# Optimization experiments

Hardware: AMD Instinct MI355X
Metric: run time of the kernel (lower is better)

Reference implementation:

```python
import jax, jax.numpy as jnp
import numpy as np
import math

N, IN_DIM, OUT_DIM = 4096, 1024, 1024
MASK = True


def setup_inputs() -> dict:
    key = jax.random.key(0)
    ks = jax.random.split(key, 6)
    s = 1.0 / math.sqrt(IN_DIM)
    return {
        "qx": jax.random.normal(ks[0], (N, IN_DIM), jnp.float32),
        "kx": jax.random.normal(ks[1], (N, IN_DIM), jnp.float32),
        "vx": jax.random.normal(ks[2], (N, IN_DIM), jnp.float32),
        # torch nn.Linear weight layout: [out_dim, in_dim], y = x @ W.T
        "Wq": jax.random.normal(ks[3], (OUT_DIM, IN_DIM), jnp.float32) * s,
        "Wk": jax.random.normal(ks[4], (OUT_DIM, IN_DIM), jnp.float32) * s,
        "Wv": jax.random.normal(ks[5], (OUT_DIM, IN_DIM), jnp.float32) * s,
    }


def reference(qx, kx, vx, Wq, Wk, Wv):
    q = qx @ Wq.T  # [n, d]
    k = kx @ Wk.T
    v = vx @ Wv.T
    scores = (q @ k.T) / jnp.float32(math.sqrt(OUT_DIM))  # [n, n]
    if MASK:
        n = qx.shape[0]
        col = jnp.arange(n)[None, :]
        row = jnp.arange(n)[:, None]
        # original: -10000 where j > i (strictly upper triangular)
        scores = scores + jnp.where(col > row, jnp.float32(-10000.0), jnp.float32(0.0))
    attn = jax.nn.softmax(scores, axis=1)
    return attn @ v
```

## Files before the change

### kernel.cpp

```cpp
#include <hip/hip_runtime.h>
#include <hip/hip_bf16.h>
#include <stdint.h>

#define NTOK 4096
#define DIM  1024

typedef unsigned short u16;
typedef __bf16 bf16x8 __attribute__((ext_vector_type(8)));
typedef float f32x4 __attribute__((ext_vector_type(4)));
typedef u16 u16x8 __attribute__((ext_vector_type(8)));

__device__ __forceinline__ u16 f2bf(float f) {
  union { float f; uint32_t u; } c; c.f = f;
  return (u16)((c.u + 0x7fffu + ((c.u >> 16) & 1u)) >> 16);
}
__device__ __forceinline__ float bf2f(u16 b) {
  union { uint32_t u; float f; } c; c.u = (uint32_t)b << 16;
  return c.f;
}

__device__ __forceinline__ float wave_max(float v) {
#pragma unroll
  for (int o = 32; o; o >>= 1) v = fmaxf(v, __shfl_xor(v, o, 64));
  return v;
}
__device__ __forceinline__ float wave_sum(float v) {
#pragma unroll
  for (int o = 32; o; o >>= 1) v += __shfl_xor(v, o, 64);
  return v;
}

__device__ __forceinline__ int xcd_swz(int orig, int nwg) {
  const int q = nwg >> 3, r = nwg & 7;
  const int x = orig & 7, i = orig >> 3;
  return (x < r ? x * (q + 1) : r * (q + 1) + (x - r) * q) + i;
}

__device__ __forceinline__ void gld16(const u16* g, u16* l) {
  __builtin_amdgcn_global_load_lds((const __attribute__((address_space(1))) void*)g,
                                   (__attribute__((address_space(3))) void*)l, 16, 0, 0);
}

__global__ __launch_bounds__(256) void cvt6(
    const float* __restrict__ qx, const float* __restrict__ kx, const float* __restrict__ vx,
    const float* __restrict__ Wq, const float* __restrict__ Wk, const float* __restrict__ Wv,
    u16* __restrict__ qxb, u16* __restrict__ kxb, u16* __restrict__ vxb,
    u16* __restrict__ Wqb, u16* __restrict__ Wkb, u16* __restrict__ Wvb)
{
  const int z = blockIdx.z;
  const int nelem = (z < 3) ? NTOK * DIM : DIM * DIM;
  const int i = (blockIdx.x * 256 + threadIdx.x) * 8;
  if (i >= nelem) return;
  const float* in = (z == 0) ? qx : (z == 1) ? kx : (z == 2) ? vx
                  : (z == 3) ? Wq : (z == 4) ? Wk : Wv;
  u16* out = (z == 0) ? qxb : (z == 1) ? kxb : (z == 2) ? vxb
           : (z == 3) ? Wqb : (z == 4) ? Wkb : Wvb;
  float4 a = *reinterpret_cast<const float4*>(in + i);
  float4 b = *reinterpret_cast<const float4*>(in + i + 4);
  u16x8 o;
  o[0] = f2bf(a.x); o[1] = f2bf(a.y); o[2] = f2bf(a.z); o[3] = f2bf(a.w);
  o[4] = f2bf(b.x); o[5] = f2bf(b.y); o[6] = f2bf(b.z); o[7] = f2bf(b.w);
  *reinterpret_cast<u16x8*>(out + i) = o;
}

template<int BM>
__device__ __forceinline__ void mm_core(
    const u16* __restrict__ A, const u16* __restrict__ B,
    int lda, int ldb, int klo, int khi, int row0, int col0,
    u16* sA, u16* sB, f32x4 (&acc)[BM / 32][4])
{
  constexpr int RPWA = BM / 4;
  constexpr int ASZ = BM * 64;
  constexpr int BSZ = 128 * 64;
  const int tid = threadIdx.x;
  const int wave = tid >> 6, lane = tid & 63;
  const int wr = wave >> 1, wc = wave & 1;
  const int l15 = lane & 15, l4 = lane >> 4;
  const int h = l15 & 7;

  const int r8 = lane >> 3;
  const int scol = ((lane & 7) ^ r8) << 3;
  const u16* gA = A + (size_t)(row0 + wave * RPWA + r8) * lda + scol;
  const u16* gB = B + (size_t)(col0 + wave * 32 + r8) * ldb + scol;
  const int lbA = wave * RPWA * 64;
  const int lbB = wave * 32 * 64;

#pragma unroll
  for (int i = 0; i < RPWA / 8; ++i)
    gld16(gA + (size_t)(i * 8) * lda + klo, &sA[lbA + i * 512]);
#pragma unroll
  for (int i = 0; i < 4; ++i)
    gld16(gB + (size_t)(i * 8) * ldb + klo, &sB[lbB + i * 512]);
  __syncthreads();

  int cur = 0;
  for (int k0 = klo; k0 < khi; k0 += 64) {
    const int nxt = cur ^ 1;
    if (k0 + 64 < khi) {
#pragma unroll
      for (int i = 0; i < RPWA / 8; ++i)
        gld16(gA + (size_t)(i * 8) * lda + k0 + 64, &sA[nxt * ASZ + lbA + i * 512]);
#pragma unroll
      for (int i = 0; i < 4; ++i)
        gld16(gB + (size_t)(i * 8) * ldb + k0 + 64, &sB[nxt * BSZ + lbB + i * 512]);
    }
    const char* bA = (const char*)(sA + cur * ASZ);
    const char* bB = (const char*)(sB + cur * BSZ);
#pragma unroll
    for (int ks = 0; ks < 2; ++ks) {
      bf16x8 af[BM / 32], bfv[4];
#pragma unroll
      for (int mf = 0; mf < BM / 32; ++mf)
        af[mf] = *reinterpret_cast<const bf16x8*>(
            bA + ((wr * (BM / 2) + mf * 16 + l15) << 7) + ((((ks << 2) + l4) ^ h) << 4));
#pragma unroll
      for (int nf = 0; nf < 4; ++nf)
        bfv[nf] = *reinterpret_cast<const bf16x8*>(
            bB + ((wc * 64 + nf * 16 + l15) << 7) + ((((ks << 2) + l4) ^ h) << 4));
#pragma unroll
      for (int mf = 0; mf < BM / 32; ++mf)
#pragma unroll
        for (int nf = 0; nf < 4; ++nf)
          acc[mf][nf] = __builtin_amdgcn_mfma_f32_16x16x32_bf16(af[mf], bfv[nf], acc[mf][nf], 0, 0, 0);
    }
    __syncthreads();
    cur = nxt;
  }
}

__global__ __launch_bounds__(256) void proj_sw(
    const u16* __restrict__ qxb, const u16* __restrict__ kxb, const u16* __restrict__ vxb,
    const u16* __restrict__ Wqb, const u16* __restrict__ Wkb, const u16* __restrict__ Wvb,
    u16* __restrict__ qb, u16* __restrict__ kb, u16* __restrict__ vT)
{
  __shared__ alignas(16) u16 sA[2 * 128 * 64];
  __shared__ alignas(16) u16 sB[2 * 128 * 64];
  const int w = xcd_swz(blockIdx.x, 768);
  const int z = w >> 8, rem = w & 255;
  const int by = rem >> 3, bx = rem & 7;
  const u16* A = (z == 0) ? qxb : (z == 1) ? kxb : vxb;
  const u16* B = (z == 0) ? Wqb : (z == 1) ? Wkb : Wvb;
  const int row0 = by * 128, col0 = bx * 128;

  f32x4 acc[4][4] = {};
  mm_core<128>(A, B, DIM, DIM, 0, DIM, row0, col0, sA, sB, acc);

  const int lane = threadIdx.x & 63;
  const int wave = threadIdx.x >> 6;
  const int l15 = lane & 15, l4 = lane >> 4;
  const int om = row0 + (wave >> 1) * 64;
  const int on = col0 + (wave & 1) * 64;
  if (z < 2) {
    u16* C = (z == 0) ? qb : kb;
#pragma unroll
    for (int mf = 0; mf < 4; ++mf)
#pragma unroll
      for (int nf = 0; nf < 4; ++nf)
#pragma unroll
        for (int r = 0; r < 4; ++r)
          C[(size_t)(om + mf * 16 + l4 * 4 + r) * DIM + (on + nf * 16 + l15)] = f2bf(acc[mf][nf][r]);
  } else {
#pragma unroll
    for (int mf = 0; mf < 4; ++mf)
#pragma unroll
      for (int nf = 0; nf < 4; ++nf) {
        ushort4 o;
        o.x = f2bf(acc[mf][nf][0]);
        o.y = f2bf(acc[mf][nf][1]);
        o.z = f2bf(acc[mf][nf][2]);
        o.w = f2bf(acc[mf][nf][3]);
        *reinterpret_cast<ushort4*>(&vT[(size_t)(on + nf * 16 + l15) * NTOK + (om + mf * 16 + l4 * 4)]) = o;
      }
  }
}

__global__ __launch_bounds__(256) void gemm_scores(
    const u16* __restrict__ A, const u16* __restrict__ B, u16* __restrict__ C, float scale)
{
  __shared__ alignas(16) u16 sA[2 * 128 * 64];
  __shared__ alignas(16) u16 sB[2 * 128 * 64];
  const int t = xcd_swz(blockIdx.x, 528);
  int by = (int)((sqrtf(8.0f * t + 1.0f) - 1.0f) * 0.5f);
  while ((by + 1) * (by + 2) / 2 <= t) ++by;
  while (by * (by + 1) / 2 > t) --by;
  const int bx = t - by * (by + 1) / 2;
  const int row0 = by * 128, col0 = bx * 128;

  f32x4 acc[4][4] = {};
  mm_core<128>(A, B, DIM, DIM, 0, DIM, row0, col0, sA, sB, acc);

  const int lane = threadIdx.x & 63;
  const int wave = threadIdx.x >> 6;
  const int l15 = lane & 15, l4 = lane >> 4;
  const int om = row0 + (wave >> 1) * 64;
  const int on = col0 + (wave & 1) * 64;
#pragma unroll
  for (int mf = 0; mf < 4; ++mf)
#pragma unroll
    for (int nf = 0; nf < 4; ++nf)
#pragma unroll
      for (int r = 0; r < 4; ++r)
        C[(size_t)(om + mf * 16 + l4 * 4 + r) * NTOK + (on + nf * 16 + l15)] = f2bf(acc[mf][nf][r] * scale);
}

__global__ __launch_bounds__(256) void gemm_pv(
    const u16* __restrict__ P, const u16* __restrict__ vT, float* __restrict__ C)
{
  __shared__ alignas(16) u16 sA[2 * 64 * 64];
  __shared__ alignas(16) u16 sB[2 * 128 * 64];
  const int w = xcd_swz(blockIdx.x, 768);
  const int bx = w & 7;
  const int cid = w >> 3;
  int by, half;
  if (cid < 32) { by = cid; half = -1; }
  else { const int j = cid - 32; by = 32 + (j >> 1); half = j & 1; }
  const int row0 = by * 64, col0 = bx * 128;
  const int Klim = row0 + 64;
  int klo = 0, khi = Klim;
  if (half >= 0) {
    const int h1 = (((Klim >> 6) + 1) >> 1) << 6;
    if (half == 0) khi = h1; else klo = h1;
  }

  f32x4 acc[2][4] = {};
  mm_core<64>(P, vT, NTOK, NTOK, klo, khi, row0, col0, sA, sB, acc);

  const int lane = threadIdx.x & 63;
  const int wave = threadIdx.x >> 6;
  const int l15 = lane & 15, l4 = lane >> 4;
  const int om = row0 + (wave >> 1) * 32;
  const int on = col0 + (wave & 1) * 64;
#pragma unroll
  for (int mf = 0; mf < 2; ++mf)
#pragma unroll
    for (int nf = 0; nf < 4; ++nf)
#pragma unroll
      for (int r = 0; r < 4; ++r) {
        const size_t idx = (size_t)(om + mf * 16 + l4 * 4 + r) * DIM + (on + nf * 16 + l15);
        if (half >= 0) atomicAdd(&C[idx], acc[mf][nf][r]);
        else C[idx] = acc[mf][nf][r];
      }
}

__global__ __launch_bounds__(256) void softmax_causal(const u16* __restrict__ S,
                                                      u16* __restrict__ P) {
  __shared__ float buf[NTOK];
  __shared__ float red[8];
  const int row = blockIdx.x;
  const int tid = threadIdx.x;
  const int limit = row + 1;
  const int limit128 = (row & ~127) + 128;
  const u16* srow = S + (size_t)row * NTOK;

  float lmax = -1e30f;
  for (int j = tid * 8; j < limit128; j += 2048) {
    float v[8];
    if (j + 8 <= limit) {
      u16x8 sv = *reinterpret_cast<const u16x8*>(srow + j);
#pragma unroll
      for (int e = 0; e < 8; ++e) v[e] = bf2f(sv[e]);
    } else {
#pragma unroll
      for (int e = 0; e < 8; ++e) v[e] = (j + e < limit) ? bf2f(srow[j + e]) : -1e30f;
    }
    float4 lo = {v[0], v[1], v[2], v[3]}, hi = {v[4], v[5], v[6], v[7]};
    *reinterpret_cast<float4*>(buf + j) = lo;
    *reinterpret_cast<float4*>(buf + j + 4) = hi;
#pragma unroll
    for (int e = 0; e < 8; ++e) lmax = fmaxf(lmax, v[e]);
  }
  lmax = wave_max(lmax);
  if ((tid & 63) == 0) red[tid >> 6] = lmax;
  __syncthreads();
  const float m = fmaxf(fmaxf(red[0], red[1]), fmaxf(red[2], red[3]));

  float lsum = 0.f;
  for (int j = tid * 8; j < limit128; j += 2048) {
    float4 lo = *reinterpret_cast<float4*>(buf + j);
    float4 hi = *reinterpret_cast<float4*>(buf + j + 4);
    float e0 = __expf(lo.x - m), e1 = __expf(lo.y - m), e2 = __expf(lo.z - m), e3 = __expf(lo.w - m);
    float e4 = __expf(hi.x - m), e5 = __expf(hi.y - m), e6 = __expf(hi.z - m), e7 = __expf(hi.w - m);
    float4 eo = {e0, e1, e2, e3}, eh = {e4, e5, e6, e7};
    *reinterpret_cast<float4*>(buf + j) = eo;
    *reinterpret_cast<float4*>(buf + j + 4) = eh;
    lsum += ((e0 + e1) + (e2 + e3)) + ((e4 + e5) + (e6 + e7));
  }
  lsum = wave_sum(lsum);
  if ((tid & 63) == 0) red[4 + (tid >> 6)] = lsum;
  __syncthreads();
  const float inv = 1.0f / (red[4] + red[5] + red[6] + red[7]);

  u16* prow = P + (size_t)row * NTOK;
  for (int j = tid * 8; j < limit128; j += 2048) {
    float4 lo = *reinterpret_cast<float4*>(buf + j);
    float4 hi = *reinterpret_cast<float4*>(buf + j + 4);
    u16x8 o;
    o[0] = f2bf(lo.x * inv); o[1] = f2bf(lo.y * inv);
    o[2] = f2bf(lo.z * inv); o[3] = f2bf(lo.w * inv);
    o[4] = f2bf(hi.x * inv); o[5] = f2bf(hi.y * inv);
    o[6] = f2bf(hi.z * inv); o[7] = f2bf(hi.w * inv);
    *reinterpret_cast<u16x8*>(prow + j) = o;
  }
}

extern "C" void kernel_launch(void* const* d_in, const int* in_sizes, int n_in,
                              void* d_out, int out_size, void* d_ws, size_t ws_size,
                              hipStream_t stream) {
  const float* qx = (const float*)d_in[0];
  const float* kx = (const float*)d_in[1];
  const float* vx = (const float*)d_in[2];
  const float* Wq = (const float*)d_in[3];
  const float* Wk = (const float*)d_in[4];
  const float* Wv = (const float*)d_in[5];
  float* out = (float*)d_out;
  char* ws = (char*)d_ws;
  const size_t MB = 1024ull * 1024ull;

  if (ws_size < 120 * MB) {
    hipMemsetAsync(d_out, 0xFF, (size_t)out_size * sizeof(float), stream);
    return;
  }

  u16* qxb = (u16*)(ws);
  u16* kxb = (u16*)(ws + 8 * MB);
  u16* vxb = (u16*)(ws + 16 * MB);
  u16* Wqb = (u16*)(ws + 24 * MB);
  u16* Wkb = (u16*)(ws + 26 * MB);
  u16* Wvb = (u16*)(ws + 28 * MB);
  u16* S   = (u16*)(ws);
  u16* qb  = (u16*)(ws + 64 * MB);
  u16* kb  = (u16*)(ws + 72 * MB);
  u16* vT  = (u16*)(ws + 80 * MB);
  u16* P   = (u16*)(ws + 88 * MB);

  hipMemsetAsync((char*)out + (size_t)2048 * DIM * 4, 0, (size_t)2048 * DIM * 4, stream);

  cvt6<<<dim3(NTOK * DIM / (256 * 8), 1, 6), 256, 0, stream>>>(
      qx, kx, vx, Wq, Wk, Wv, qxb, kxb, vxb, Wqb, Wkb, Wvb);

  proj_sw<<<768, 256, 0, stream>>>(qxb, kxb, vxb, Wqb, Wkb, Wvb, qb, kb, vT);

  gemm_scores<<<528, 256, 0, stream>>>(qb, kb, S, 0.03125f);

  softmax_causal<<<NTOK, 256, 0, stream>>>(S, P);

  gemm_pv<<<768, 256, 0, stream>>>(P, vT, out);
}
```

Measured before the change: 140.5 us.

## Switch GEMM mainloop to 3-stage K=32 pipeline with vmcnt-based waits

```diff
diff --git a/kernel.cpp b/kernel.cpp
--- a/kernel.cpp
+++ b/kernel.cpp
@@ -39,6 +39,14 @@
 __device__ __forceinline__ void gld16(const u16* g, u16* l) {
   __builtin_amdgcn_global_load_lds((const __attribute__((address_space(1))) void*)g,
                                    (__attribute__((address_space(3))) void*)l, 16, 0, 0);
+}
+
+template<int N> __device__ __forceinline__ void wait_vmcnt() {
+  if constexpr (N == 0) asm volatile("s_waitcnt vmcnt(0)" ::: "memory");
+  else if constexpr (N == 3) asm volatile("s_waitcnt vmcnt(3)" ::: "memory");
+  else if constexpr (N == 4) asm volatile("s_waitcnt vmcnt(4)" ::: "memory");
+  else if constexpr (N == 6) asm volatile("s_waitcnt vmcnt(6)" ::: "memory");
+  else if constexpr (N == 8) asm volatile("s_waitcnt vmcnt(8)" ::: "memory");
 }
 
 __global__ __launch_bounds__(256) void cvt6(
@@ -67,64 +75,72 @@
 __device__ __forceinline__ void mm_core(
     const u16* __restrict__ A, const u16* __restrict__ B,
     int lda, int ldb, int klo, int khi, int row0, int col0,
-    u16* sA, u16* sB, f32x4 (&acc)[BM / 32][4])
-{
-  constexpr int RPWA = BM / 4;
-  constexpr int ASZ = BM * 64;
-  constexpr int BSZ = 128 * 64;
+    u16* lds, f32x4 (&acc)[BM / 32][4])
+{
+  constexpr int ABUF = BM * 32;
+  constexpr int BUFSZ = ABUF + 128 * 32;
+  constexpr int RPW_A = BM / 4;
+  constexpr int LPS = BM / 64 + 2;
   const int tid = threadIdx.x;
   const int wave = tid >> 6, lane = tid & 63;
   const int wr = wave >> 1, wc = wave & 1;
   const int l15 = lane & 15, l4 = lane >> 4;
-  const int h = l15 & 7;
-
-  const int r8 = lane >> 3;
-  const int scol = ((lane & 7) ^ r8) << 3;
-  const u16* gA = A + (size_t)(row0 + wave * RPWA + r8) * lda + scol;
-  const u16* gB = B + (size_t)(col0 + wave * 32 + r8) * ldb + scol;
-  const int lbA = wave * RPWA * 64;
-  const int lbB = wave * 32 * 64;
-
-#pragma unroll
-  for (int i = 0; i < RPWA / 8; ++i)
-    gld16(gA + (size_t)(i * 8) * lda + klo, &sA[lbA + i * 512]);
-#pragma unroll
-  for (int i = 0; i < 4; ++i)
-    gld16(gB + (size_t)(i * 8) * ldb + klo, &sB[lbB + i * 512]);
-  __syncthreads();
+
+  const int srow = lane >> 2;
+  const int gchunk = ((lane & 3) ^ ((lane >> 3) & 3)) << 3;
+  const u16* gA = A + (size_t)(row0 + wave * RPW_A + srow) * lda + gchunk;
+  const u16* gB = B + (size_t)(col0 + wave * 32 + srow) * ldb + gchunk;
+  const int lbA = wave * RPW_A * 32;
+  const int lbB = ABUF + wave * 32 * 32;
+
+  const int nsteps = (khi - klo) >> 5;
+
+  auto stage = [&](int s, u16* buf) {
+    const int k = klo + (s << 5);
+#pragma unroll
+    for (int i = 0; i < RPW_A / 16; ++i)
+      gld16(gA + (size_t)(i * 16) * lda + k, buf + lbA + i * 16 * 32);
+#pragma unroll
+    for (int i = 0; i < 2; ++i)
+      gld16(gB + (size_t)(i * 16) * ldb + k, buf + lbB + i * 16 * 32);
+  };
+
+  if (0 < nsteps) stage(0, lds);
+  if (1 < nsteps) stage(1, lds + BUFSZ);
+  if (2 < nsteps) stage(2, lds + 2 * BUFSZ);
 
   int cur = 0;
-  for (int k0 = klo; k0 < khi; k0 += 64) {
-    const int nxt = cur ^ 1;
-    if (k0 + 64 < khi) {
-#pragma unroll
-      for (int i = 0; i < RPWA / 8; ++i)
-        gld16(gA + (size_t)(i * 8) * lda + k0 + 64, &sA[nxt * ASZ + lbA + i * 512]);
-#pragma unroll
-      for (int i = 0; i < 4; ++i)
-        gld16(gB + (size_t)(i * 8) * ldb + k0 + 64, &sB[nxt * BSZ + lbB + i * 512]);
+  for (int t = 0; t < nsteps; ++t) {
+    const int ahead = nsteps - 1 - t;
+    if (ahead >= 2)      wait_vmcnt<2 * LPS>();
+    else if (ahead == 1) wait_vmcnt<LPS>();
+    else                 wait_vmcnt<0>();
+    __builtin_amdgcn_s_barrier();
+    __builtin_amdgcn_sched_barrier(0);
+    const char* buf = (const char*)(lds + cur * BUFSZ);
+
+    bf16x8 af[BM / 32], bfv[4];
+#pragma unroll
+    for (int mf = 0; mf < BM / 32; ++mf) {
+      const int r = wr * (BM / 2) + mf * 16 + l15;
+      af[mf] = *reinterpret_cast<const bf16x8*>(
+          buf + (r << 6) + (((l4 ^ (r >> 1)) & 3) << 4));
     }
-    const char* bA = (const char*)(sA + cur * ASZ);
-    const char* bB = (const char*)(sB + cur * BSZ);
-#pragma unroll
-    for (int ks = 0; ks < 2; ++ks) {
-      bf16x8 af[BM / 32], bfv[4];
-#pragma unroll
-      for (int mf = 0; mf < BM / 32; ++mf)
-        af[mf] = *reinterpret_cast<const bf16x8*>(
-            bA + ((wr * (BM / 2) + mf * 16 + l15) << 7) + ((((ks << 2) + l4) ^ h) << 4));
+#pragma unroll
+    for (int nf = 0; nf < 4; ++nf) {
+      const int r = wc * 64 + nf * 16 + l15;
+      bfv[nf] = *reinterpret_cast<const bf16x8*>(
+          buf + 2 * ABUF + (r << 6) + (((l4 ^ (r >> 1)) & 3) << 4));
+    }
+#pragma unroll
+    for (int mf = 0; mf < BM / 32; ++mf)
 #pragma unroll
       for (int nf = 0; nf < 4; ++nf)
-        bfv[nf] = *reinterpret_cast<const bf16x8*>(
-            bB + ((wc * 64 + nf * 16 + l15) << 7) + ((((ks << 2) + l4) ^ h) << 4));
-#pragma unroll
-      for (int mf = 0; mf < BM / 32; ++mf)
-#pragma unroll
-        for (int nf = 0; nf < 4; ++nf)
-          acc[mf][nf] = __builtin_amdgcn_mfma_f32_16x16x32_bf16(af[mf], bfv[nf], acc[mf][nf], 0, 0, 0);
-    }
-    __syncthreads();
-    cur = nxt;
+        acc[mf][nf] = __builtin_amdgcn_mfma_f32_16x16x32_bf16(af[mf], bfv[nf], acc[mf][nf], 0, 0, 0);
+
+    __builtin_amdgcn_s_barrier();
+    if (t + 3 < nsteps) stage(t + 3, lds + cur * BUFSZ);
+    cur = (cur == 2) ? 0 : cur + 1;
   }
 }
 
@@ -133,8 +149,7 @@
     const u16* __restrict__ Wqb, const u16* __restrict__ Wkb, const u16* __restrict__ Wvb,
     u16* __restrict__ qb, u16* __restrict__ kb, u16* __restrict__ vT)
 {
-  __shared__ alignas(16) u16 sA[2 * 128 * 64];
-  __shared__ alignas(16) u16 sB[2 * 128 * 64];
+  __shared__ alignas(16) u16 lds[3 * 256 * 32];
   const int w = xcd_swz(blockIdx.x, 768);
   const int z = w >> 8, rem = w & 255;
   const int by = rem >> 3, bx = rem & 7;
@@ -143,7 +158,7 @@
   const int row0 = by * 128, col0 = bx * 128;
 
   f32x4 acc[4][4] = {};
-  mm_core<128>(A, B, DIM, DIM, 0, DIM, row0, col0, sA, sB, acc);
+  mm_core<128>(A, B, DIM, DIM, 0, DIM, row0, col0, lds, acc);
 
   const int lane = threadIdx.x & 63;
   const int wave = threadIdx.x >> 6;
@@ -177,8 +192,7 @@
 __global__ __launch_bounds__(256) void gemm_scores(
     const u16* __restrict__ A, const u16* __restrict__ B, u16* __restrict__ C, float scale)
 {
-  __shared__ alignas(16) u16 sA[2 * 128 * 64];
-  __shared__ alignas(16) u16 sB[2 * 128 * 64];
+  __shared__ alignas(16) u16 lds[3 * 256 * 32];
   const int t = xcd_swz(blockIdx.x, 528);
   int by = (int)((sqrtf(8.0f * t + 1.0f) - 1.0f) * 0.5f);
   while ((by + 1) * (by + 2) / 2 <= t) ++by;
@@ -187,7 +201,7 @@
   const int row0 = by * 128, col0 = bx * 128;
 
   f32x4 acc[4][4] = {};
-  mm_core<128>(A, B, DIM, DIM, 0, DIM, row0, col0, sA, sB, acc);
+  mm_core<128>(A, B, DIM, DIM, 0, DIM, row0, col0, lds, acc);
 
   const int lane = threadIdx.x & 63;
   const int wave = threadIdx.x >> 6;
@@ -206,8 +220,7 @@
 __global__ __launch_bounds__(256) void gemm_pv(
     const u16* __restrict__ P, const u16* __restrict__ vT, float* __restrict__ C)
 {
-  __shared__ alignas(16) u16 sA[2 * 64 * 64];
-  __shared__ alignas(16) u16 sB[2 * 128 * 64];
+  __shared__ alignas(16) u16 lds[3 * 192 * 32];
   const int w = xcd_swz(blockIdx.x, 768);
   const int bx = w & 7;
   const int cid = w >> 3;
@@ -223,7 +236,7 @@
   }
 
   f32x4 acc[2][4] = {};
-  mm_core<64>(P, vT, NTOK, NTOK, klo, khi, row0, col0, sA, sB, acc);
+  mm_core<64>(P, vT, NTOK, NTOK, klo, khi, row0, col0, lds, acc);
 
   const int lane = threadIdx.x & 63;
   const int wave = threadIdx.x >> 6;
```

Measured after the change: 141.5 us. About the same (+0.7%).
